# Kernel optimization log

Measured on AMD Instinct MI355X. Metric: run time of the kernel, lower is better.

The kernel has to match this reference:

```python
import jax, jax.numpy as jnp
import numpy as np

NUM_NODES = 1_000_000
IN_DIM, HID = 128, 256
B = 4096                 # edges per batch (src/pos/neg each B)
N2 = 3 * B               # seed nodes
FAN = 10
N1 = N2 * FAN            # hop-1 nodes
N0 = N1 * FAN            # hop-0 nodes


def setup_inputs() -> dict:
    key = jax.random.key(0)
    ks = jax.random.split(key, 16)
    g = lambda k, shp, scale: jax.random.normal(k, shp, dtype=jnp.float32) * scale
    return {
        "node_feat": g(ks[0], (NUM_NODES, IN_DIM), 1.0),
        "gids0": jax.random.randint(ks[1], (N0,), 0, NUM_NODES, dtype=jnp.int32),
        "neigh_idx0": jax.random.randint(ks[2], (N1, FAN), 0, N0, dtype=jnp.int32),
        "neigh_idx1": jax.random.randint(ks[3], (N2, FAN), 0, N1, dtype=jnp.int32),
        "W_self0": g(ks[4], (IN_DIM, HID), (1.0 / IN_DIM) ** 0.5),
        "W_neigh0": g(ks[5], (IN_DIM, HID), (1.0 / IN_DIM) ** 0.5),
        "b0": jnp.zeros((HID,), jnp.float32),
        "W_self1": g(ks[6], (HID, HID), (1.0 / HID) ** 0.5),
        "W_neigh1": g(ks[7], (HID, HID), (1.0 / HID) ** 0.5),
        "b1": jnp.zeros((HID,), jnp.float32),
        "Wp1": g(ks[8], (HID, HID), (1.0 / HID) ** 0.5),
        "bp1": jnp.zeros((HID,), jnp.float32),
        "Wp2": g(ks[9], (HID, HID), (1.0 / HID) ** 0.5),
        "bp2": jnp.zeros((HID,), jnp.float32),
        "Wp3": g(ks[10], (HID, 1), (1.0 / HID) ** 0.5),
        "bp3": jnp.zeros((1,), jnp.float32),
    }


def _sage(x, n_dst, neigh, Ws, Wn, b):
    # x: [n_src, d]; neigh: [n_dst, fan] local indices into x
    x_dst = x[:n_dst]                       # dst nodes are a prefix of src nodes
    agg = jnp.mean(x[neigh], axis=1)        # [n_dst, d] mean aggregation
    return x_dst @ Ws + agg @ Wn + b


def reference(node_feat, gids0, neigh_idx0, neigh_idx1,
              W_self0, W_neigh0, b0, W_self1, W_neigh1, b1,
              Wp1, bp1, Wp2, bp2, Wp3, bp3):
    # embedding gather for the full sampled neighborhood
    x = node_feat[gids0]                                    # [N0, IN_DIM]
    h = jax.nn.relu(_sage(x, N1, neigh_idx0, W_self0, W_neigh0, b0))  # [N1, HID]
    h = _sage(h, N2, neigh_idx1, W_self1, W_neigh1, b1)     # [N2, HID]
    src, pos, neg = h[:B], h[B:2 * B], h[2 * B:3 * B]
    # predictor on elementwise product of endpoint embeddings
    z = jnp.concatenate([src, src], axis=0) * jnp.concatenate([pos, neg], axis=0)
    z = jax.nn.relu(z @ Wp1 + bp1)
    z = jax.nn.relu(z @ Wp2 + bp2)
    scores = z @ Wp3 + bp3                                  # [2B, 1]
    return scores
```

## Files before the change

### kernel.cpp

```cpp
#include <hip/hip_runtime.h>
#include <hip/hip_bf16.h>

#define NNODES 1000000
#define INDIM  128
#define HIDC   256
#define BSZ    4096
#define N2C    12288
#define FANC   10
#define N1C    122880
#define N0C    1228800

typedef __bf16 bf16_t;
typedef bf16_t bf16x2 __attribute__((ext_vector_type(2)));
typedef bf16_t bf16x4 __attribute__((ext_vector_type(4)));
typedef bf16_t bf16x8 __attribute__((ext_vector_type(8)));
typedef float  f32x4  __attribute__((ext_vector_type(4)));

__global__ __launch_bounds__(256) void prep_all(const float* __restrict__ Ws0,
                                                const float* __restrict__ Wn0,
                                                const float* __restrict__ Ws1,
                                                const float* __restrict__ Wn1,
                                                const float* __restrict__ Wp1,
                                                const float* __restrict__ Wp2,
                                                bf16_t* __restrict__ Wt0,
                                                bf16_t* __restrict__ Wt1,
                                                bf16_t* __restrict__ WtP1,
                                                bf16_t* __restrict__ WtP2) {
  int t = blockIdx.x * 256 + threadIdx.x;
  if (t < 65536) {
    int n = t >> 8, k = t & 255;
    float v = (k < 128) ? Ws0[k * 256 + n] : Wn0[(k - 128) * 256 + n];
    Wt0[t] = (bf16_t)v;
  } else if (t < 196608) {
    int u = t - 65536; int n = u >> 9, k = u & 511;
    float v = (k < 256) ? Ws1[k * 256 + n] : Wn1[(k - 256) * 256 + n];
    Wt1[u] = (bf16_t)v;
  } else if (t < 262144) {
    int u = t - 196608; int n = u >> 8, k = u & 255;
    WtP1[u] = (bf16_t)Wp1[k * 256 + n];
  } else {
    int u = t - 262144; int n = u >> 8, k = u & 255;
    WtP2[u] = (bf16_t)Wp2[k * 256 + n];
  }
}

#define LDA0 264
__global__ __launch_bounds__(256) void fused0(const float* __restrict__ feat,
                                              const int* __restrict__ gids,
                                              const int* __restrict__ nidx,
                                              const bf16_t* __restrict__ Wt,
                                              const float* __restrict__ bias,
                                              bf16_t* __restrict__ h) {
  __shared__ __align__(16) bf16_t As[64 * LDA0];
  __shared__ int nid_s[64 * FANC];
  __shared__ int self_s[64];
  int tid = threadIdx.x;
  int m0 = blockIdx.x * 64;

  for (int t = tid; t < 64 * FANC; t += 256)
    nid_s[t] = gids[nidx[(size_t)m0 * FANC + t]];
  if (tid < 64) self_s[tid] = gids[m0 + tid];
  __syncthreads();

  int wv = tid >> 6, lane = tid & 63;
  const float2* f2 = (const float2*)feat;
  for (int i = 0; i < 16; i++) {
    int d = wv * 16 + i;
    float ax = 0.f, ay = 0.f;
#pragma unroll
    for (int j = 0; j < FANC; j++) {
      int nd = nid_s[d * FANC + j];
      float2 v = f2[(size_t)nd * 64 + lane];
      ax += v.x; ay += v.y;
    }
    int sn = self_s[d];
    float2 xs = f2[(size_t)sn * 64 + lane];
    bf16_t* row = As + d * LDA0;
    bf16x2 w0 = { (bf16_t)xs.x, (bf16_t)xs.y };
    *(bf16x2*)(row + lane * 2) = w0;
    bf16x2 w1 = { (bf16_t)(ax * 0.1f), (bf16_t)(ay * 0.1f) };
    *(bf16x2*)(row + 128 + lane * 2) = w1;
  }
  __syncthreads();

  int l15 = lane & 15, quad = lane >> 4;
  int n0 = wv * 64;
  f32x4 acc[4][4] = {};
  for (int k0 = 0; k0 < 256; k0 += 32) {
    bf16x8 a[4], b[4];
#pragma unroll
    for (int mt = 0; mt < 4; mt++)
      a[mt] = *(const bf16x8*)(As + (mt * 16 + l15) * LDA0 + k0 + quad * 8);
#pragma unroll
    for (int nt = 0; nt < 4; nt++)
      b[nt] = *(const bf16x8*)(Wt + (size_t)(n0 + nt * 16 + l15) * 256 + k0 + quad * 8);
#pragma unroll
    for (int mt = 0; mt < 4; mt++)
#pragma unroll
      for (int nt = 0; nt < 4; nt++)
        acc[mt][nt] = __builtin_amdgcn_mfma_f32_16x16x32_bf16(a[mt], b[nt], acc[mt][nt], 0, 0, 0);
  }
#pragma unroll
  for (int mt = 0; mt < 4; mt++)
#pragma unroll
    for (int nt = 0; nt < 4; nt++) {
      int col = n0 + nt * 16 + l15;
      float bv = bias[col];
#pragma unroll
      for (int r = 0; r < 4; r++) {
        int row = m0 + mt * 16 + quad * 4 + r;
        float v = fmaxf(acc[mt][nt][r] + bv, 0.f);
        h[(size_t)row * 256 + col] = (bf16_t)v;
      }
    }
}

#define LDA1 520
__global__ __launch_bounds__(256) void fused1(const bf16_t* __restrict__ h,
                                              const int* __restrict__ nidx,
                                              const bf16_t* __restrict__ Wt,
                                              const float* __restrict__ bias,
                                              float* __restrict__ h2) {
  __shared__ __align__(16) bf16_t As[32 * LDA1];
  __shared__ int nid_s[32 * FANC];
  int tid = threadIdx.x;
  int m0 = blockIdx.x * 32;

  for (int t = tid; t < 32 * FANC; t += 256)
    nid_s[t] = nidx[(size_t)m0 * FANC + t];
  __syncthreads();

  int wv = tid >> 6, lane = tid & 63;
  const bf16x4* h4 = (const bf16x4*)h;
  for (int i = 0; i < 8; i++) {
    int d = wv * 8 + i;
    float a0 = 0.f, a1 = 0.f, a2 = 0.f, a3 = 0.f;
#pragma unroll
    for (int j = 0; j < FANC; j++) {
      int nd = nid_s[d * FANC + j];
      bf16x4 v = h4[(size_t)nd * 64 + lane];
      a0 += (float)v[0]; a1 += (float)v[1]; a2 += (float)v[2]; a3 += (float)v[3];
    }
    bf16x4 xs = h4[(size_t)(m0 + d) * 64 + lane];
    bf16_t* row = As + d * LDA1;
    *(bf16x4*)(row + lane * 4) = xs;
    bf16x4 ag = { (bf16_t)(a0 * 0.1f), (bf16_t)(a1 * 0.1f),
                  (bf16_t)(a2 * 0.1f), (bf16_t)(a3 * 0.1f) };
    *(bf16x4*)(row + 256 + lane * 4) = ag;
  }
  __syncthreads();

  int l15 = lane & 15, quad = lane >> 4;
  int n0 = wv * 64;
  f32x4 acc[2][4] = {};
  for (int k0 = 0; k0 < 512; k0 += 32) {
    bf16x8 a[2], b[4];
#pragma unroll
    for (int mt = 0; mt < 2; mt++)
      a[mt] = *(const bf16x8*)(As + (mt * 16 + l15) * LDA1 + k0 + quad * 8);
#pragma unroll
    for (int nt = 0; nt < 4; nt++)
      b[nt] = *(const bf16x8*)(Wt + (size_t)(n0 + nt * 16 + l15) * 512 + k0 + quad * 8);
#pragma unroll
    for (int mt = 0; mt < 2; mt++)
#pragma unroll
      for (int nt = 0; nt < 4; nt++)
        acc[mt][nt] = __builtin_amdgcn_mfma_f32_16x16x32_bf16(a[mt], b[nt], acc[mt][nt], 0, 0, 0);
  }
#pragma unroll
  for (int mt = 0; mt < 2; mt++)
#pragma unroll
    for (int nt = 0; nt < 4; nt++) {
      int col = n0 + nt * 16 + l15;
      float bv = bias[col];
#pragma unroll
      for (int r = 0; r < 4; r++) {
        int row = m0 + mt * 16 + quad * 4 + r;
        h2[(size_t)row * 256 + col] = acc[mt][nt][r] + bv;
      }
    }
}

#define LDP 264
__device__ __forceinline__ void gemm_tile_lds(const bf16_t* __restrict__ Asrc,
                                              const bf16_t* __restrict__ Wt,
                                              const float* __restrict__ bias,
                                              bf16_t* __restrict__ Dst,
                                              int wv, int lane) {
  int l15 = lane & 15, quad = lane >> 4;
  int n0 = wv * 64;
  f32x4 acc[4][4] = {};
  for (int k0 = 0; k0 < 256; k0 += 32) {
    bf16x8 a[4], b[4];
#pragma unroll
    for (int mt = 0; mt < 4; mt++)
      a[mt] = *(const bf16x8*)(Asrc + (mt * 16 + l15) * LDP + k0 + quad * 8);
#pragma unroll
    for (int nt = 0; nt < 4; nt++)
      b[nt] = *(const bf16x8*)(Wt + (size_t)(n0 + nt * 16 + l15) * 256 + k0 + quad * 8);
#pragma unroll
    for (int mt = 0; mt < 4; mt++)
#pragma unroll
      for (int nt = 0; nt < 4; nt++)
        acc[mt][nt] = __builtin_amdgcn_mfma_f32_16x16x32_bf16(a[mt], b[nt], acc[mt][nt], 0, 0, 0);
  }
#pragma unroll
  for (int mt = 0; mt < 4; mt++)
#pragma unroll
    for (int nt = 0; nt < 4; nt++) {
      int col = n0 + nt * 16 + l15;
      float bv = bias[col];
#pragma unroll
      for (int r = 0; r < 4; r++) {
        int row = mt * 16 + quad * 4 + r;
        Dst[row * LDP + col] = (bf16_t)fmaxf(acc[mt][nt][r] + bv, 0.f);
      }
    }
}

__global__ __launch_bounds__(256) void pred_fused(const float* __restrict__ h2,
                                                  const bf16_t* __restrict__ WtP1,
                                                  const float* __restrict__ bp1,
                                                  const bf16_t* __restrict__ WtP2,
                                                  const float* __restrict__ bp2,
                                                  const float* __restrict__ Wp3,
                                                  const float* __restrict__ bp3,
                                                  float* __restrict__ out) {
  __shared__ __align__(16) bf16_t Z0[64 * LDP];
  __shared__ __align__(16) bf16_t Z1[64 * LDP];
  int tid = threadIdx.x, wv = tid >> 6, lane = tid & 63;
  int m0 = blockIdx.x * 64;

  for (int i = 0; i < 16; i++) {
    int rl = wv * 16 + i;
    int r = m0 + rl;
    int a = r & 4095, b = r + 4096;
    float4 va = *(const float4*)(h2 + (size_t)a * 256 + lane * 4);
    float4 vb = *(const float4*)(h2 + (size_t)b * 256 + lane * 4);
    bf16x4 o = { (bf16_t)(va.x * vb.x), (bf16_t)(va.y * vb.y),
                 (bf16_t)(va.z * vb.z), (bf16_t)(va.w * vb.w) };
    *(bf16x4*)(Z0 + rl * LDP + lane * 4) = o;
  }
  __syncthreads();

  gemm_tile_lds(Z0, WtP1, bp1, Z1, wv, lane);
  __syncthreads();
  gemm_tile_lds(Z1, WtP2, bp2, Z0, wv, lane);
  __syncthreads();

  float4 w = *(const float4*)(Wp3 + lane * 4);
  float b3 = bp3[0];
  for (int i = 0; i < 16; i++) {
    int rl = wv * 16 + i;
    bf16x4 v = *(const bf16x4*)(Z0 + rl * LDP + lane * 4);
    float s = (float)v[0] * w.x + (float)v[1] * w.y + (float)v[2] * w.z + (float)v[3] * w.w;
    for (int off = 32; off > 0; off >>= 1) s += __shfl_down(s, off);
    if (lane == 0) out[m0 + rl] = s + b3;
  }
}

extern "C" void kernel_launch(void* const* d_in, const int* in_sizes, int n_in,
                              void* d_out, int out_size, void* d_ws, size_t ws_size,
                              hipStream_t stream) {
  const float* node_feat = (const float*)d_in[0];
  const int*   gids0     = (const int*)d_in[1];
  const int*   nidx0     = (const int*)d_in[2];
  const int*   nidx1     = (const int*)d_in[3];
  const float* Wself0    = (const float*)d_in[4];
  const float* Wneigh0   = (const float*)d_in[5];
  const float* b0        = (const float*)d_in[6];
  const float* Wself1    = (const float*)d_in[7];
  const float* Wneigh1   = (const float*)d_in[8];
  const float* b1        = (const float*)d_in[9];
  const float* Wp1       = (const float*)d_in[10];
  const float* bp1       = (const float*)d_in[11];
  const float* Wp2       = (const float*)d_in[12];
  const float* bp2       = (const float*)d_in[13];
  const float* Wp3       = (const float*)d_in[14];
  const float* bp3       = (const float*)d_in[15];

  char* ws = (char*)d_ws;
  bf16_t* Wt0  = (bf16_t*)(ws + 0);
  bf16_t* Wt1  = (bf16_t*)(ws + (128 << 10));
  bf16_t* WtP1 = (bf16_t*)(ws + (384 << 10));
  bf16_t* WtP2 = (bf16_t*)(ws + (512 << 10));
  char* big = ws + (1 << 20);
  bf16_t* h  = (bf16_t*)big;
  float*  h2 = (float*)(big + (64ULL << 20));
  float* out = (float*)d_out;

  prep_all<<<1280, 256, 0, stream>>>(Wself0, Wneigh0, Wself1, Wneigh1, Wp1, Wp2,
                                     Wt0, Wt1, WtP1, WtP2);

  fused0<<<N1C / 64, 256, 0, stream>>>(node_feat, gids0, nidx0, Wt0, b0, h);

  fused1<<<N2C / 32, 256, 0, stream>>>(h, nidx1, Wt1, b1, h2);

  pred_fused<<<8192 / 64, 256, 0, stream>>>(h2, WtP1, bp1, WtP2, bp2, Wp3, bp3, out);
}
```

Measured before the change: 742.3 us.

## Widen fused0 gathers to float4 with half-wave neighbor split; store h2 as bf16

The fused0 gather is restructured so each half-wave loads 16-byte float4 chunks of a 128-float row. The two halves split the 10 neighbors of two destination rows at once and are combined with a cross-half shuffle, aiming for fewer, wider random memory transactions and more loads in flight. Separately, the layer-1 output h2 is written and read as bf16 instead of fp32, halving that intermediate's traffic into the predictor kernel. The cost is extra shuffles and a further precision reduction in the final embeddings.

```diff
diff --git a/kernel.cpp b/kernel.cpp
--- a/kernel.cpp
+++ b/kernel.cpp
@@ -63,23 +63,35 @@
   __syncthreads();
 
   int wv = tid >> 6, lane = tid & 63;
-  const float2* f2 = (const float2*)feat;
-  for (int i = 0; i < 16; i++) {
-    int d = wv * 16 + i;
-    float ax = 0.f, ay = 0.f;
-#pragma unroll
-    for (int j = 0; j < FANC; j++) {
-      int nd = nid_s[d * FANC + j];
-      float2 v = f2[(size_t)nd * 64 + lane];
-      ax += v.x; ay += v.y;
-    }
-    int sn = self_s[d];
-    float2 xs = f2[(size_t)sn * 64 + lane];
-    bf16_t* row = As + d * LDA0;
-    bf16x2 w0 = { (bf16_t)xs.x, (bf16_t)xs.y };
-    *(bf16x2*)(row + lane * 2) = w0;
-    bf16x2 w1 = { (bf16_t)(ax * 0.1f), (bf16_t)(ay * 0.1f) };
-    *(bf16x2*)(row + 128 + lane * 2) = w1;
+  int half = lane >> 5, l31 = lane & 31;
+  const float4* f4 = (const float4*)feat;
+  for (int p = 0; p < 8; p++) {
+    int d = wv * 16 + p * 2;
+    f32x4 accA = {0.f, 0.f, 0.f, 0.f};
+    f32x4 accB = {0.f, 0.f, 0.f, 0.f};
+#pragma unroll
+    for (int k = 0; k < 5; k++) {
+      int ndA = nid_s[d * FANC + 2 * k + half];
+      float4 vA = f4[(size_t)ndA * 32 + l31];
+      accA.x += vA.x; accA.y += vA.y; accA.z += vA.z; accA.w += vA.w;
+      int ndB = nid_s[(d + 1) * FANC + 2 * k + half];
+      float4 vB = f4[(size_t)ndB * 32 + l31];
+      accB.x += vB.x; accB.y += vB.y; accB.z += vB.z; accB.w += vB.w;
+    }
+    accA.x += __shfl_xor(accA.x, 32); accA.y += __shfl_xor(accA.y, 32);
+    accA.z += __shfl_xor(accA.z, 32); accA.w += __shfl_xor(accA.w, 32);
+    accB.x += __shfl_xor(accB.x, 32); accB.y += __shfl_xor(accB.y, 32);
+    accB.z += __shfl_xor(accB.z, 32); accB.w += __shfl_xor(accB.w, 32);
+    int sn = self_s[d + half];
+    float4 xs = f4[(size_t)sn * 32 + l31];
+    int dw = d + half;
+    bf16_t* row = As + dw * LDA0;
+    bf16x4 w0 = { (bf16_t)xs.x, (bf16_t)xs.y, (bf16_t)xs.z, (bf16_t)xs.w };
+    *(bf16x4*)(row + l31 * 4) = w0;
+    f32x4 ag = half ? accB : accA;
+    bf16x4 w1 = { (bf16_t)(ag.x * 0.1f), (bf16_t)(ag.y * 0.1f),
+                  (bf16_t)(ag.z * 0.1f), (bf16_t)(ag.w * 0.1f) };
+    *(bf16x4*)(row + 128 + l31 * 4) = w1;
   }
   __syncthreads();
 
@@ -120,7 +132,7 @@
                                               const int* __restrict__ nidx,
                                               const bf16_t* __restrict__ Wt,
                                               const float* __restrict__ bias,
-                                              float* __restrict__ h2) {
+                                              bf16_t* __restrict__ h2) {
   __shared__ __align__(16) bf16_t As[32 * LDA1];
   __shared__ int nid_s[32 * FANC];
   int tid = threadIdx.x;
@@ -176,7 +188,7 @@
 #pragma unroll
       for (int r = 0; r < 4; r++) {
         int row = m0 + mt * 16 + quad * 4 + r;
-        h2[(size_t)row * 256 + col] = acc[mt][nt][r] + bv;
+        h2[(size_t)row * 256 + col] = (bf16_t)(acc[mt][nt][r] + bv);
       }
     }
 }
@@ -218,7 +230,7 @@
     }
 }
 
-__global__ __launch_bounds__(256) void pred_fused(const float* __restrict__ h2,
+__global__ __launch_bounds__(256) void pred_fused(const bf16_t* __restrict__ h2,
                                                   const bf16_t* __restrict__ WtP1,
                                                   const float* __restrict__ bp1,
                                                   const bf16_t* __restrict__ WtP2,
@@ -235,10 +247,12 @@
     int rl = wv * 16 + i;
     int r = m0 + rl;
     int a = r & 4095, b = r + 4096;
-    float4 va = *(const float4*)(h2 + (size_t)a * 256 + lane * 4);
-    float4 vb = *(const float4*)(h2 + (size_t)b * 256 + lane * 4);
-    bf16x4 o = { (bf16_t)(va.x * vb.x), (bf16_t)(va.y * vb.y),
-                 (bf16_t)(va.z * vb.z), (bf16_t)(va.w * vb.w) };
+    bf16x4 va = *(const bf16x4*)(h2 + (size_t)a * 256 + lane * 4);
+    bf16x4 vb = *(const bf16x4*)(h2 + (size_t)b * 256 + lane * 4);
+    bf16x4 o = { (bf16_t)((float)va[0] * (float)vb[0]),
+                 (bf16_t)((float)va[1] * (float)vb[1]),
+                 (bf16_t)((float)va[2] * (float)vb[2]),
+                 (bf16_t)((float)va[3] * (float)vb[3]) };
     *(bf16x4*)(Z0 + rl * LDP + lane * 4) = o;
   }
   __syncthreads();
@@ -286,7 +300,7 @@
   bf16_t* WtP2 = (bf16_t*)(ws + (512 << 10));
   char* big = ws + (1 << 20);
   bf16_t* h  = (bf16_t*)big;
-  float*  h2 = (float*)(big + (64ULL << 20));
+  bf16_t* h2 = (bf16_t*)(big + (64ULL << 20));
   float* out = (float*)d_out;
 
   prep_all<<<1280, 256, 0, stream>>>(Wself0, Wneigh0, Wself1, Wneigh1, Wp1, Wp2,
```

Result: slower. 760.7 us (+2.5%).
